# Performance work log

Hardware: AMD Instinct MI355X
Metric: run time of the kernel (lower is better)

## Reference

```python
import jax, jax.numpy as jnp
import numpy as np

FEATURES = [3, 64, 128, 256]
N_ITER = 5  # NNMF multiplicative-update iterations
K = 3
PAD = K // 2  # 'same' padding so spatial dims are preserved inside a block
EPS = 1e-20
BN_EPS = 1e-5


def conv2d(x, w, pad):
    # x: [B, Cin, H, W], w: [Cout, Cin, kh, kw] (torch OIHW layout)
    return jax.lax.conv_general_dilated(
        x, w, window_strides=(1, 1),
        padding=[(pad, pad), (pad, pad)],
        dimension_numbers=("NCHW", "OIHW", "NCHW"))


def nnmf_conv2d(x, w, n_iter, pad):
    # Non-negative, L1-normalized weights (per output filter)
    wp = jnp.abs(w)
    wn = wp / (wp.sum(axis=(1, 2, 3), keepdims=True) + EPS)
    # Input is non-negative (ReLU applied upstream); L1-normalize over channels
    x = x / (x.sum(axis=1, keepdims=True) + EPS)
    b, _, hh, ww = x.shape
    c_out = w.shape[0]
    # h init: uniform distribution over output channels
    h = jnp.full((b, c_out, hh, ww), 1.0 / c_out, dtype=x.dtype)
    # conv_transpose2d(h, W, padding=pad) == conv2d(h, flip(W).swap(O,I), padding=k-1-pad);
    # with odd k and pad = k//2 this is again 'same' padding.
    wt = jnp.transpose(jnp.flip(wn, (2, 3)), (1, 0, 2, 3))  # [Cin, Cout, kh, kw] as OIHW
    for _ in range(n_iter):
        recon = conv2d(h, wt, pad)                    # [B, Cin, H, W]
        h = h * conv2d(x / (recon + EPS), wn, pad)    # multiplicative update
        h = h / (h.sum(axis=1, keepdims=True) + EPS)  # renormalize over channels
    return h


def batchnorm(x, gamma, beta):
    # Training-mode BN: batch statistics over (N, H, W), biased variance
    mean = x.mean(axis=(0, 2, 3), keepdims=True)
    var = x.var(axis=(0, 2, 3), keepdims=True)
    xn = (x - mean) * jax.lax.rsqrt(var + BN_EPS)
    return xn * gamma[None, :, None, None] + beta[None, :, None, None]


def avgpool2(x):
    b, c, h, w = x.shape
    return x.reshape(b, c, h // 2, 2, w // 2, 2).mean(axis=(3, 5))


def block(x, w_nnmf, w_conv, b_conv, gamma, beta):
    x = jax.nn.relu(x)
    h = nnmf_conv2d(x, w_nnmf, N_ITER, PAD)
    y = conv2d(h, w_conv, 0) + b_conv[None, :, None, None]  # 1x1 conv
    y = jax.nn.relu(y)
    y = batchnorm(y, gamma, beta)
    return avgpool2(y)


def setup_inputs() -> dict:
    key = jax.random.key(0)
    keys = jax.random.split(key, 7)
    inp = {"x": jax.random.normal(keys[0], (16, 3, 128, 128), jnp.float32)}
    for i in range(3):
        cin, cout = FEATURES[i], FEATURES[i + 1]
        inp[f"w_nnmf{i}"] = jax.random.uniform(keys[1 + 2 * i], (cout, cin, K, K), jnp.float32)
        inp[f"w_conv{i}"] = jax.random.normal(keys[2 + 2 * i], (cout, cout, 1, 1), jnp.float32) / np.sqrt(cout).astype(np.float32)
        inp[f"b_conv{i}"] = jnp.zeros((cout,), jnp.float32)
        inp[f"gamma{i}"] = jnp.ones((cout,), jnp.float32)
        inp[f"beta{i}"] = jnp.zeros((cout,), jnp.float32)
    return inp


def reference(x, w_nnmf0, w_conv0, b_conv0, gamma0, beta0,
              w_nnmf1, w_conv1, b_conv1, gamma1, beta1,
              w_nnmf2, w_conv2, b_conv2, gamma2, beta2):
    x = block(x, w_nnmf0, w_conv0, b_conv0, gamma0, beta0)
    x = block(x, w_nnmf1, w_conv1, b_conv1, gamma1, beta1)
    x = block(x, w_nnmf2, w_conv2, b_conv2, gamma2, beta2)
    return x  # [16, 256, 16, 16]
```

## Files before the change

### kernel.cpp

```cpp
#include <hip/hip_runtime.h>

#define EPSV  1e-20f
#define BNEPS 1e-5f

typedef _Float16 f16x8 __attribute__((ext_vector_type(8)));
typedef _Float16 f16x4 __attribute__((ext_vector_type(4)));
typedef float    f32x4 __attribute__((ext_vector_type(4)));

__device__ inline unsigned pack2f16(float a, float b) {
    unsigned short ua = __builtin_bit_cast(unsigned short, (_Float16)a);
    unsigned short ub = __builtin_bit_cast(unsigned short, (_Float16)b);
    return ((unsigned)ub << 16) | ua;
}

template<int CIN, int COUT>
__global__ __launch_bounds__(256) void prep_w_f16_kernel(const float* __restrict__ w,
                                                         _Float16* __restrict__ wAh,
                                                         _Float16* __restrict__ wBh)
{
    const int co  = blockIdx.x;
    const int tid = threadIdx.x;
    const int N   = CIN * 9;
    const float* wrow = w + (size_t)co * N;

    float s = 0.f;
    for (int i = tid; i < N; i += 256) s += fabsf(wrow[i]);
    __shared__ float red[4];
    #pragma unroll
    for (int m = 32; m; m >>= 1) s += __shfl_xor(s, m, 64);
    if ((tid & 63) == 0) red[tid >> 6] = s;
    __syncthreads();
    s = red[0] + red[1] + red[2] + red[3];
    const float rn = 1.f / (s + EPSV);

    for (int i = tid; i < N; i += 256) {
        const int ci = i / 9, tap = i % 9;
        const int ky = tap / 3, kx = tap % 3;
        const float v = fabsf(wrow[i]) * rn;
        const int tf = (2 - ky) * 3 + (2 - kx);
        wBh[(((size_t)(ci >> 5) * 9 + tap) * COUT + co) * 32 + (ci & 31)] = (_Float16)v;
        wAh[(((size_t)(co >> 5) * 9 + tf) * CIN + ci) * 32 + (co & 31)] = (_Float16)v;
    }
}

__global__ __launch_bounds__(256) void zero_f16_kernel(_Float16* __restrict__ a, int n)
{
    const int i = blockIdx.x * 256 + threadIdx.x;
    if (i < n) a[i] = (_Float16)0.f;
}

__global__ __launch_bounds__(64) void prep_w0_kernel(const float* __restrict__ w,
                                                     _Float16* __restrict__ wA0h,
                                                     _Float16* __restrict__ wB0h)
{
    const int co = blockIdx.x, tid = threadIdx.x;
    float s = (tid < 27) ? fabsf(w[co * 27 + tid]) : 0.f;
    #pragma unroll
    for (int m = 32; m; m >>= 1) s += __shfl_xor(s, m, 64);
    const float rn = 1.f / (s + EPSV);
    if (tid < 27) {
        const int ci = tid / 9, tap = tid % 9, ky = tap / 3, kx = tap % 3;
        const float v = fabsf(w[co * 27 + tid]) * rn;
        const int tf = (2 - ky) * 3 + (2 - kx);
        wB0h[co * 64 + tap * 4 + ci] = (_Float16)v;
        wA0h[(((co >> 5) * 9 + tf) * 16 + ci) * 32 + (co & 31)] = (_Float16)v;
    }
}

__global__ __launch_bounds__(256) void prep_w1h_kernel(const float* __restrict__ w1,
                                                       _Float16* __restrict__ w1h, int n)
{
    const int i = blockIdx.x * 256 + threadIdx.x;
    if (i < n) w1h[i] = (_Float16)w1[i];
}

__global__ __launch_bounds__(256) void xn0_kernel(const float* __restrict__ x,
                                                  _Float16* __restrict__ xn4,
                                                  int npx, int HW)
{
    const int p = blockIdx.x * 256 + threadIdx.x;
    if (p >= npx) return;
    const int b = p / HW, r = p % HW;
    const float* ip = x + (size_t)b * 3 * HW + r;
    const float v0 = fmaxf(ip[0], 0.f), v1 = fmaxf(ip[HW], 0.f), v2 = fmaxf(ip[2 * HW], 0.f);
    const float rs = 1.f / (v0 + v1 + v2 + EPSV);
    unsigned* d = (unsigned*)(xn4 + (size_t)p * 4);
    d[0] = pack2f16(v0 * rs, v1 * rs);
    d[1] = pack2f16(v2 * rs, 0.f);
}

template<int ICg, int OCg, int NSPLIT, int OST, int NW, int NSIN,
         bool NORM_IN, bool UPDATE, bool FIRST>
__global__ __launch_bounds__(256, 1) void mfconv5(
    const _Float16* __restrict__ in, const _Float16* __restrict__ wgt,
    const _Float16* __restrict__ aux, _Float16* __restrict__ out,
    const float* __restrict__ Sin, float* __restrict__ Sout,
    int H, int W, int sstride)
{
    constexpr bool CSTAGE = FIRST && NORM_IN;
    constexpr int OCWG = OCg / NSPLIT;
    constexpr int NF = OCWG / 16;
    constexpr int HS = 18, WSp = 18, NSP = HS * WSp;
    constexpr int ICP = 40;
    constexpr int NCH = ICg / 32;
    constexpr int LS = (NSPLIT == 4) ? 2 : (NSPLIT == 2) ? 1 : 0;
    constexpr int NLD = NSP * 4;
    constexpr int IREG = (NLD + 255) / 256;
    constexpr int WOC = OCWG * 32;
    constexpr int NWLD = 9 * OCWG * 4;
    constexpr int WREG = (NWLD + 255) / 256;
    static_assert(OCWG % 16 == 0 && ICg % 32 == 0, "cfg");

    __shared__ _Float16 in_t[CSTAGE ? 1 : 2][NSP * ICP];
    __shared__ _Float16 w_t[2][9 * WOC];
    __shared__ float rS[(NORM_IN && !FIRST) ? NSP : 1];

    const int tid = threadIdx.x;
    const int lane = tid & 63, wave = tid >> 6;
    const int kq = lane >> 4, l15 = lane & 15;
    const int split = blockIdx.x & (NSPLIT - 1);
    const int tx = blockIdx.x >> LS;
    const int x0 = tx * 16, y0 = blockIdx.y * 16, b = blockIdx.z;
    const int HW = H * W;
    const int oc0 = split * OCWG;

    f16x8 ild[CSTAGE ? 1 : IREG];
    f16x8 wld[WREG];

    auto iload = [&](int kc) {
        #pragma unroll
        for (int r = 0; r < IREG; ++r) {
            const int i = tid + r * 256;
            f16x8 v = {0, 0, 0, 0, 0, 0, 0, 0};
            if (i < NLD) {
                const int sp = i >> 2, seg = i & 3;
                const int yy = y0 + sp / WSp - 1, xx = x0 + sp % WSp - 1;
                if (yy >= 0 && yy < H && xx >= 0 && xx < W)
                    v = __builtin_nontemporal_load((const f16x8*)(in +
                        ((size_t)b * HW + (size_t)yy * W + xx) * ICg + kc * 32 + seg * 8));
            }
            ild[r] = v;
        }
    };
    auto wload = [&](int kc) {
        #pragma unroll
        for (int r = 0; r < WREG; ++r) {
            const int j = tid + r * 256;
            if (j < NWLD) {
                const int tap = j / (OCWG * 4), rem = j % (OCWG * 4);
                const int oc = rem >> 2, e = rem & 3;
                wld[r] = *(const f16x8*)(wgt +
                    (((size_t)kc * 9 + tap) * OCg + oc0 + oc) * 32 + e * 8);
            }
        }
    };
    auto iwrite = [&](int buf) {
        #pragma unroll
        for (int r = 0; r < IREG; ++r) {
            const int i = tid + r * 256;
            if (i < NLD) {
                const int sp = i >> 2, seg = i & 3;
                if constexpr (NORM_IN && !FIRST) {
                    const float f = rS[sp];
                    unsigned* d = (unsigned*)&in_t[buf][sp * ICP + seg * 8];
                    d[0] = pack2f16((float)ild[r][0] * f, (float)ild[r][1] * f);
                    d[1] = pack2f16((float)ild[r][2] * f, (float)ild[r][3] * f);
                    d[2] = pack2f16((float)ild[r][4] * f, (float)ild[r][5] * f);
                    d[3] = pack2f16((float)ild[r][6] * f, (float)ild[r][7] * f);
                } else {
                    *(f16x8*)&in_t[buf][sp * ICP + seg * 8] = ild[r];
                }
            }
        }
    };
    auto wwrite = [&](int buf) {
        #pragma unroll
        for (int r = 0; r < WREG; ++r) {
            const int j = tid + r * 256;
            if (j < NWLD) {
                const int tap = j / (OCWG * 4), rem = j % (OCWG * 4);
                const int oc = rem >> 2, e = rem & 3;
                const int slot = e ^ ((oc >> 1) & 3);
                *(f16x8*)&w_t[buf][tap * WOC + oc * 32 + slot * 8] = wld[r];
            }
        }
    };

    const int prow = wave * 4;

    f32x4 acc[4][NF];
    #pragma unroll
    for (int mf = 0; mf < 4; ++mf)
        #pragma unroll
        for (int nf = 0; nf < NF; ++nf) acc[mf][nf] = (f32x4){0.f, 0.f, 0.f, 0.f};

    if constexpr (!CSTAGE) iload(0);
    wload(0);
    if constexpr (NORM_IN && !FIRST) {
        for (int i = tid; i < NSP; i += 256) {
            const int yy = y0 + i / WSp - 1, xx = x0 + i % WSp - 1;
            float sv = 0.f;
            if (yy >= 0 && yy < H && xx >= 0 && xx < W) {
                const size_t pix = (size_t)b * HW + (size_t)yy * W + xx;
                #pragma unroll
                for (int k = 0; k < NSIN; ++k) sv += Sin[(size_t)k * sstride + pix];
            }
            rS[i] = 1.f / (sv + EPSV);
        }
        __syncthreads();
    }
    if constexpr (CSTAGE) {
        const unsigned cpk = pack2f16(1.0f / (float)ICg, 1.0f / (float)ICg);
        for (int i = tid; i < NSP; i += 256) {
            const int yy = y0 + i / WSp - 1, xx = x0 + i % WSp - 1;
            const bool ok = (yy >= 0 && yy < H && xx >= 0 && xx < W);
            unsigned* d = (unsigned*)&in_t[0][i * ICP];
            #pragma unroll
            for (int seg = 0; seg < 16; ++seg) d[seg] = ok ? cpk : 0u;
        }
    } else {
        iwrite(0);
    }
    wwrite(0);
    __syncthreads();

    int cur = 0;
    for (int kc = 0; kc < NCH; ++kc) {
        if (kc + 1 < NCH) {
            if constexpr (!CSTAGE) iload(kc + 1);
            wload(kc + 1);
        }
        {
            const _Float16* ib = &in_t[CSTAGE ? 0 : cur][0];
            const _Float16* wb = &w_t[cur][0];
            #pragma unroll
            for (int dy = 0; dy < 3; ++dy) {
                #pragma unroll
                for (int dx = 0; dx < 3; ++dx) {
                    const int tap = dy * 3 + dx;
                    f16x8 bfr[NF];
                    #pragma unroll
                    for (int nf = 0; nf < NF; ++nf) {
                        const int oc = nf * 16 + l15;
                        bfr[nf] = *(const f16x8*)(
                            wb + tap * WOC + oc * 32 + (kq ^ ((oc >> 1) & 3)) * 8);
                    }
                    f16x8 afr[4];
                    #pragma unroll
                    for (int mf = 0; mf < 4; ++mf)
                        afr[mf] = *(const f16x8*)(
                            ib + ((prow + mf + dy) * WSp + l15 + dx) * ICP + kq * 8);
                    #pragma unroll
                    for (int mf = 0; mf < 4; ++mf)
                        #pragma unroll
                        for (int nf = 0; nf < NF; ++nf)
                            acc[mf][nf] = __builtin_amdgcn_mfma_f32_16x16x32_f16(
                                afr[mf], bfr[nf], acc[mf][nf], 0, 0, 0);
                }
            }
        }
        if (kc + 1 < NCH) {
            if constexpr (!CSTAGE) iwrite(cur ^ 1);
            wwrite(cur ^ 1);
            __syncthreads();
            cur ^= 1;
        }
    }

    #pragma unroll
    for (int mf = 0; mf < 4; ++mf) {
        const int gy = y0 + prow + mf;
        const size_t pixbase = (size_t)b * HW + (size_t)gy * W + x0 + kq * 4;
        if constexpr (!UPDATE) {
            #pragma unroll
            for (int nf = 0; nf < NF; ++nf) {
                const int oc = oc0 + nf * 16 + l15;
                if (oc < NW) {
                    #pragma unroll
                    for (int r = 0; r < 4; ++r) {
                        const size_t idx = (pixbase + r) * OST + oc;
                        out[idx] = (_Float16)((float)aux[idx] / (acc[mf][nf][r] + EPSV));
                    }
                }
            }
        } else {
            float s[4] = {0.f, 0.f, 0.f, 0.f};
            #pragma unroll
            for (int nf = 0; nf < NF; ++nf) {
                const int oc = oc0 + nf * 16 + l15;
                #pragma unroll
                for (int r = 0; r < 4; ++r) {
                    const size_t idx = (pixbase + r) * OST + oc;
                    float hv;
                    if constexpr (FIRST) hv = acc[mf][nf][r];
                    else                 hv = (float)out[idx] * acc[mf][nf][r];
                    const _Float16 hq = (_Float16)hv;
                    out[idx] = hq;
                    s[r] += (float)hq;
                }
            }
            #pragma unroll
            for (int mm = 1; mm < 16; mm <<= 1) {
                #pragma unroll
                for (int r = 0; r < 4; ++r) s[r] += __shfl_xor(s[r], mm);
            }
            if (l15 == 0) {
                float* sp_ = Sout + (size_t)split * sstride + pixbase;
                sp_[0] = s[0]; sp_[1] = s[1]; sp_[2] = s[2]; sp_[3] = s[3];
            }
        }
    }
}

template<bool FIRST>
__global__ __launch_bounds__(256) void mf0u_kernel(
    const _Float16* __restrict__ ratio4, const _Float16* __restrict__ wB0h,
    _Float16* __restrict__ h, float* __restrict__ Sout, int H, int W)
{
    constexpr int TW = 16;
    __shared__ _Float16 a_t[64 * 72];

    const int tid = threadIdx.x;
    const int lane = tid & 63, wave = tid >> 6;
    const int kq = lane >> 4, l15 = lane & 15;
    const int x0 = blockIdx.x * TW, y0 = blockIdx.y * 4, b = blockIdx.z;
    const int HW = H * W;

    for (int i = tid; i < 64 * 72 / 2; i += 256) ((unsigned*)a_t)[i] = 0;
    __syncthreads();
    for (int i = tid; i < 576; i += 256) {
        const int px = i / 9, tap = i % 9;
        const int py = px / TW, pxx = px % TW;
        const int yy = y0 + py + tap / 3 - 1, xx = x0 + pxx + tap % 3 - 1;
        if (yy >= 0 && yy < H && xx >= 0 && xx < W)
            *(f16x4*)&a_t[px * 72 + tap * 4] =
                *(const f16x4*)(ratio4 + ((size_t)b * HW + (size_t)yy * W + xx) * 4);
    }
    __syncthreads();

    f32x4 acc[4];
    #pragma unroll
    for (int nf = 0; nf < 4; ++nf) acc[nf] = (f32x4){0.f, 0.f, 0.f, 0.f};
    #pragma unroll
    for (int kc = 0; kc < 2; ++kc) {
        const f16x8 afr = *(const f16x8*)&a_t[(wave * 16 + l15) * 72 + kc * 32 + kq * 8];
        #pragma unroll
        for (int nf = 0; nf < 4; ++nf) {
            const f16x8 bfr = *(const f16x8*)(wB0h + (size_t)(nf * 16 + l15) * 64 + kc * 32 + kq * 8);
            acc[nf] = __builtin_amdgcn_mfma_f32_16x16x32_f16(afr, bfr, acc[nf], 0, 0, 0);
        }
    }

    const int pl = wave * 16 + kq * 4;
    const size_t pixbase = (size_t)b * HW + (size_t)(y0 + pl / TW) * W + x0 + pl % TW;
    float s[4] = {0.f, 0.f, 0.f, 0.f};
    #pragma unroll
    for (int nf = 0; nf < 4; ++nf) {
        const int oc = nf * 16 + l15;
        #pragma unroll
        for (int r = 0; r < 4; ++r) {
            const size_t idx = (pixbase + r) * 64 + oc;
            float hv;
            if constexpr (FIRST) hv = acc[nf][r];
            else                 hv = (float)h[idx] * acc[nf][r];
            const _Float16 hq = (_Float16)hv;
            h[idx] = hq;
            s[r] += (float)hq;
        }
    }
    #pragma unroll
    for (int mm = 1; mm < 16; mm <<= 1) {
        #pragma unroll
        for (int r = 0; r < 4; ++r) s[r] += __shfl_xor(s[r], mm);
    }
    if (l15 == 0) {
        float* sp_ = Sout + pixbase;
        sp_[0] = s[0]; sp_[1] = s[1]; sp_[2] = s[2]; sp_[3] = s[3];
    }
}

template<int C, int MODE, int NSIN>
__global__ __launch_bounds__(256) void posty_kernel(
    const _Float16* __restrict__ h, const float* __restrict__ S,
    const _Float16* __restrict__ w1h, const float* __restrict__ bias,
    const float* __restrict__ bnst, float* __restrict__ part,
    void* __restrict__ outp, int H, int W, int sst)
{
    constexpr int NF = C / 16, CP = C + 8;
    __shared__ _Float16 a_t[64 * CP];
    __shared__ float rs_t[64];
    __shared__ float sred1[MODE == 0 ? 4 * C : 1];
    __shared__ float sred2[MODE == 0 ? 4 * C : 1];
    __shared__ float pool_t[MODE == 1 ? 16 * (C + 1) : 1];

    const int tid = threadIdx.x;
    const int lane = tid & 63, wave = tid >> 6;
    const int kq = lane >> 4, l15 = lane & 15;
    const int WT = W / 32;
    const int tx = blockIdx.x % WT, ty = blockIdx.x / WT;
    const int b = blockIdx.y;
    const int HW = H * W;

    if (tid < 64) {
        const int gp = (2 * ty + (tid >> 5)) * W + tx * 32 + (tid & 31);
        float sv = 0.f;
        #pragma unroll
        for (int k = 0; k < NSIN; ++k) sv += S[(size_t)k * sst + (size_t)b * HW + gp];
        rs_t[tid] = 1.f / (sv + EPSV);
    }
    __syncthreads();
    for (int i = tid; i < 64 * (C / 8); i += 256) {
        const int sp = i / (C / 8), seg = i % (C / 8);
        const int gp = (2 * ty + (sp >> 5)) * W + tx * 32 + (sp & 31);
        const f16x8 v = *(const f16x8*)(h + ((size_t)b * HW + gp) * C + seg * 8);
        const float f = rs_t[sp];
        unsigned* d = (unsigned*)&a_t[sp * CP + seg * 8];
        d[0] = pack2f16((float)v[0] * f, (float)v[1] * f);
        d[1] = pack2f16((float)v[2] * f, (float)v[3] * f);
        d[2] = pack2f16((float)v[4] * f, (float)v[5] * f);
        d[3] = pack2f16((float)v[6] * f, (float)v[7] * f);
    }
    __syncthreads();

    f32x4 acc[NF];
    #pragma unroll
    for (int nf = 0; nf < NF; ++nf) acc[nf] = (f32x4){0.f, 0.f, 0.f, 0.f};
    #pragma unroll
    for (int kc = 0; kc < C / 32; ++kc) {
        const f16x8 afr = *(const f16x8*)&a_t[(wave * 16 + l15) * CP + kc * 32 + kq * 8];
        #pragma unroll
        for (int nf = 0; nf < NF; ++nf) {
            const f16x8 bfr = *(const f16x8*)(w1h + (size_t)(nf * 16 + l15) * C + kc * 32 + kq * 8);
            acc[nf] = __builtin_amdgcn_mfma_f32_16x16x32_f16(afr, bfr, acc[nf], 0, 0, 0);
        }
    }

    const int pl = wave * 16 + kq * 4;

    if constexpr (MODE == 0) {
        const int wgid = b * gridDim.x + blockIdx.x;
        #pragma unroll
        for (int nf = 0; nf < NF; ++nf) {
            const int oc = nf * 16 + l15;
            const float bv = bias[oc];
            float s1 = 0.f, s2 = 0.f;
            #pragma unroll
            for (int r = 0; r < 4; ++r) {
                const float y = fmaxf(acc[nf][r] + bv, 0.f);
                s1 += y; s2 += y * y;
            }
            s1 += __shfl_xor(s1, 16); s2 += __shfl_xor(s2, 16);
            s1 += __shfl_xor(s1, 32); s2 += __shfl_xor(s2, 32);
            if (kq == 0) {
                sred1[wave * C + oc] = s1;
                sred2[wave * C + oc] = s2;
            }
        }
        __syncthreads();
        for (int oc = tid; oc < C; oc += 256) {
            const float s1 = sred1[oc] + sred1[C + oc] + sred1[2 * C + oc] + sred1[3 * C + oc];
            const float s2 = sred2[oc] + sred2[C + oc] + sred2[2 * C + oc] + sred2[3 * C + oc];
            part[((size_t)wgid * C + oc) * 2 + 0] = s1;
            part[((size_t)wgid * C + oc) * 2 + 1] = s2;
        }
    } else {
        __syncthreads();
        #pragma unroll
        for (int nf = 0; nf < NF; ++nf) {
            const int oc = nf * 16 + l15;
            const float bv = bias[oc];
            #pragma unroll
            for (int r = 0; r < 4; ++r)
                a_t[(pl + r) * CP + oc] = (_Float16)fmaxf(acc[nf][r] + bv, 0.f);
        }
        __syncthreads();
        const int Wo = W >> 1;
        if constexpr (MODE == 2) {
            for (int i = tid; i < 16 * C; i += 256) {
                const int ox = i % 16, c = i / 16;
                const float y00 = (float)a_t[(2 * ox) * CP + c];
                const float y01 = (float)a_t[(2 * ox + 1) * CP + c];
                const float y10 = (float)a_t[(32 + 2 * ox) * CP + c];
                const float y11 = (float)a_t[(32 + 2 * ox + 1) * CP + c];
                const float v = (y00 + y01 + y10 + y11) * 0.25f * bnst[c] + bnst[C + c];
                ((float*)outp)[(((size_t)b * C + c) * (size_t)(H >> 1) + ty) * Wo + tx * 16 + ox] = v;
            }
        } else {
            for (int i = tid; i < 16 * C; i += 256) {
                const int ox = i / C, c = i % C;
                const float y00 = (float)a_t[(2 * ox) * CP + c];
                const float y01 = (float)a_t[(2 * ox + 1) * CP + c];
                const float y10 = (float)a_t[(32 + 2 * ox) * CP + c];
                const float y11 = (float)a_t[(32 + 2 * ox + 1) * CP + c];
                pool_t[ox * (C + 1) + c] =
                    fmaxf((y00 + y01 + y10 + y11) * 0.25f * bnst[c] + bnst[C + c], 0.f);
            }
            __syncthreads();
            const int px = tid >> 4, prt = tid & 15;
            float ps = 0.f;
            for (int c = prt; c < C; c += 16) ps += pool_t[px * (C + 1) + c];
            ps += __shfl_xor(ps, 1); ps += __shfl_xor(ps, 2);
            ps += __shfl_xor(ps, 4); ps += __shfl_xor(ps, 8);
            const float rs = 1.f / (ps + EPSV);
            _Float16* xo = (_Float16*)outp;
            const size_t obase = ((size_t)b * (HW >> 2) + (size_t)ty * Wo + tx * 16 + px) * C;
            for (int c = prt; c < C; c += 16)
                xo[obase + c] = (_Float16)(pool_t[px * (C + 1) + c] * rs);
        }
    }
}

template<int C>
__global__ __launch_bounds__(256) void stats_kernel(const float* __restrict__ part, int nwg, float invM,
                                                    const float* __restrict__ gamma,
                                                    const float* __restrict__ beta,
                                                    float* __restrict__ stats)
{
    const int oc = blockIdx.x;
    const int tid = threadIdx.x;
    float s1 = 0.f, s2 = 0.f;
    for (int w = tid; w < nwg; w += 256) {
        s1 += part[((size_t)w * C + oc) * 2 + 0];
        s2 += part[((size_t)w * C + oc) * 2 + 1];
    }
    __shared__ float r1[4], r2[4];
    #pragma unroll
    for (int m = 32; m; m >>= 1) { s1 += __shfl_xor(s1, m, 64); s2 += __shfl_xor(s2, m, 64); }
    if ((tid & 63) == 0) { r1[tid >> 6] = s1; r2[tid >> 6] = s2; }
    __syncthreads();
    if (tid == 0) {
        s1 = r1[0] + r1[1] + r1[2] + r1[3];
        s2 = r2[0] + r2[1] + r2[2] + r2[3];
        const float mean = s1 * invM;
        const float var  = s2 * invM - mean * mean;
        const float rstd = rsqrtf(var + BNEPS);
        const float scale = gamma[oc] * rstd;
        stats[oc]     = scale;
        stats[C + oc] = beta[oc] - mean * scale;
    }
}

extern "C" void kernel_launch(void* const* d_in, const int* in_sizes, int n_in,
                              void* d_out, int out_size, void* d_ws, size_t ws_size,
                              hipStream_t stream)
{
    const float* x = (const float*)d_in[0];
    float* ws      = (float*)d_ws;
    float* S       = ws;
    float* part    = S + 262144;
    float* bnstats = part + 1048576;
    _Float16* h      = (_Float16*)(bnstats + 512);
    _Float16* xnh    = h + 16777216;
    _Float16* ratioh = xnh + 4194304;
    _Float16* wAh    = ratioh + 4194304;
    _Float16* wBh    = wAh + 294912;
    _Float16* w1h    = wBh + 294912;
    _Float16* wA0h   = w1h + 65536;
    _Float16* wB0h   = wA0h + 9216;

    const int B = 16;

    {
        const int H = 128, W = 128, HW = H * W, npx = B * HW;
        zero_f16_kernel<<<(9216 + 255) / 256, 256, 0, stream>>>(wA0h, 9216);
        prep_w0_kernel<<<64, 64, 0, stream>>>((const float*)d_in[1], wA0h, wB0h);
        xn0_kernel<<<npx / 256, 256, 0, stream>>>(x, xnh, npx, HW);
        mfconv5<64, 16, 1, 4, 4, 1, true, false, true>
            <<<dim3(8, 8, B), 256, 0, stream>>>(h, wA0h, xnh, ratioh, S, nullptr, H, W, npx);
        mf0u_kernel<true><<<dim3(8, 32, B), 256, 0, stream>>>(ratioh, wB0h, h, S, H, W);
        for (int it = 1; it < 5; ++it) {
            mfconv5<64, 16, 1, 4, 4, 1, true, false, false>
                <<<dim3(8, 8, B), 256, 0, stream>>>(h, wA0h, xnh, ratioh, S, nullptr, H, W, npx);
            mf0u_kernel<false><<<dim3(8, 32, B), 256, 0, stream>>>(ratioh, wB0h, h, S, H, W);
        }
        prep_w1h_kernel<<<16, 256, 0, stream>>>((const float*)d_in[2], w1h, 64 * 64);
        dim3 pg((W / 32) * (H / 2), B);
        posty_kernel<64, 0, 1><<<pg, 256, 0, stream>>>(h, S, w1h, (const float*)d_in[3],
                                                       nullptr, part, nullptr, H, W, npx);
        stats_kernel<64><<<64, 256, 0, stream>>>(part, pg.x * pg.y, 1.0f / (float)npx,
                                                 (const float*)d_in[4], (const float*)d_in[5], bnstats);
        posty_kernel<64, 1, 1><<<pg, 256, 0, stream>>>(h, S, w1h, (const float*)d_in[3],
                                                       bnstats, nullptr, xnh, H, W, npx);
    }

    {
        const int H = 64, W = 64, HW = H * W, npx = B * HW;
        prep_w_f16_kernel<64, 128><<<128, 256, 0, stream>>>((const float*)d_in[6], wAh, wBh);
        mfconv5<128, 64, 1, 64, 64, 1, true, false, true>
            <<<dim3(4, 4, B), 256, 0, stream>>>(h, wAh, xnh, ratioh, S, nullptr, H, W, npx);
        mfconv5<64, 128, 2, 128, 128, 1, false, true, true>
            <<<dim3(8, 4, B), 256, 0, stream>>>(ratioh, wBh, nullptr, h, nullptr, S, H, W, npx);
        for (int it = 1; it < 5; ++it) {
            mfconv5<128, 64, 1, 64, 64, 2, true, false, false>
                <<<dim3(4, 4, B), 256, 0, stream>>>(h, wAh, xnh, ratioh, S, nullptr, H, W, npx);
            mfconv5<64, 128, 2, 128, 128, 1, false, true, false>
                <<<dim3(8, 4, B), 256, 0, stream>>>(ratioh, wBh, nullptr, h, nullptr, S, H, W, npx);
        }
        prep_w1h_kernel<<<64, 256, 0, stream>>>((const float*)d_in[7], w1h, 128 * 128);
        dim3 pg((W / 32) * (H / 2), B);
        posty_kernel<128, 0, 2><<<pg, 256, 0, stream>>>(h, S, w1h, (const float*)d_in[8],
                                                        nullptr, part, nullptr, H, W, npx);
        stats_kernel<128><<<128, 256, 0, stream>>>(part, pg.x * pg.y, 1.0f / (float)npx,
                                                   (const float*)d_in[9], (const float*)d_in[10], bnstats);
        posty_kernel<128, 1, 2><<<pg, 256, 0, stream>>>(h, S, w1h, (const float*)d_in[8],
                                                        bnstats, nullptr, xnh, H, W, npx);
    }

    {
        const int H = 32, W = 32, HW = H * W, npx = B * HW;
        prep_w_f16_kernel<128, 256><<<256, 256, 0, stream>>>((const float*)d_in[11], wAh, wBh);
        mfconv5<256, 128, 4, 128, 128, 1, true, false, true>
            <<<dim3(8, 2, B), 256, 0, stream>>>(h, wAh, xnh, ratioh, S, nullptr, H, W, npx);
        mfconv5<128, 256, 4, 256, 256, 1, false, true, true>
            <<<dim3(8, 2, B), 256, 0, stream>>>(ratioh, wBh, nullptr, h, nullptr, S, H, W, npx);
        for (int it = 1; it < 5; ++it) {
            mfconv5<256, 128, 4, 128, 128, 4, true, false, false>
                <<<dim3(8, 2, B), 256, 0, stream>>>(h, wAh, xnh, ratioh, S, nullptr, H, W, npx);
            mfconv5<128, 256, 4, 256, 256, 1, false, true, false>
                <<<dim3(8, 2, B), 256, 0, stream>>>(ratioh, wBh, nullptr, h, nullptr, S, H, W, npx);
        }
        prep_w1h_kernel<<<256, 256, 0, stream>>>((const float*)d_in[12], w1h, 256 * 256);
        dim3 pg((W / 32) * (H / 2), B);
        posty_kernel<256, 0, 4><<<pg, 256, 0, stream>>>(h, S, w1h, (const float*)d_in[13],
                                                        nullptr, part, nullptr, H, W, npx);
        stats_kernel<256><<<256, 256, 0, stream>>>(part, pg.x * pg.y, 1.0f / (float)npx,
                                                   (const float*)d_in[14], (const float*)d_in[15], bnstats);
        posty_kernel<256, 2, 4><<<pg, 256, 0, stream>>>(h, S, w1h, (const float*)d_in[13],
                                                        bnstats, nullptr, d_out, H, W, npx);
    }
}
```

Measured before the change: 824.7 us.

## Fuse NNMF reconstruction and update convs into one halo-tiled kernel per iteration

Adds mffuse_kernel, which computes the reconstruction conv over a 20x20 haloed tile, forms the ratio x/recon in LDS, then runs the update conv and h renormalisation sums in the same kernel. This removes the ratio round-trip through global memory and halves launches for blocks 0 and 1. It also merges all weight preparation into one kernel and changes the block-2 reconstruction split. The cost is recomputing recon on the halo ring, plus heavy LDS and register use at one block per CU.

```diff
diff --git a/kernel.cpp b/kernel.cpp
--- a/kernel.cpp
+++ b/kernel.cpp
@@ -13,26 +13,20 @@
     return ((unsigned)ub << 16) | ua;
 }
 
-template<int CIN, int COUT>
-__global__ __launch_bounds__(256) void prep_w_f16_kernel(const float* __restrict__ w,
-                                                         _Float16* __restrict__ wAh,
-                                                         _Float16* __restrict__ wBh)
+__device__ __forceinline__ void prep_generic(const float* __restrict__ w, int CIN, int COUT,
+                                             _Float16* __restrict__ wAh, _Float16* __restrict__ wBh,
+                                             int co, int tid, float* red)
 {
-    const int co  = blockIdx.x;
-    const int tid = threadIdx.x;
-    const int N   = CIN * 9;
+    const int N = CIN * 9;
     const float* wrow = w + (size_t)co * N;
-
     float s = 0.f;
     for (int i = tid; i < N; i += 256) s += fabsf(wrow[i]);
-    __shared__ float red[4];
     #pragma unroll
     for (int m = 32; m; m >>= 1) s += __shfl_xor(s, m, 64);
     if ((tid & 63) == 0) red[tid >> 6] = s;
     __syncthreads();
     s = red[0] + red[1] + red[2] + red[3];
     const float rn = 1.f / (s + EPSV);
-
     for (int i = tid; i < N; i += 256) {
         const int ci = i / 9, tap = i % 9;
         const int ky = tap / 3, kx = tap % 3;
@@ -43,35 +37,51 @@
     }
 }
 
-__global__ __launch_bounds__(256) void zero_f16_kernel(_Float16* __restrict__ a, int n)
+__global__ __launch_bounds__(256) void prep_all_kernel(
+    const float* __restrict__ w0,  const float* __restrict__ w1_0,
+    const float* __restrict__ wb1, const float* __restrict__ w1_1,
+    const float* __restrict__ wb2, const float* __restrict__ w1_2,
+    _Float16* __restrict__ wA0h, _Float16* __restrict__ wB0h,
+    _Float16* __restrict__ wA1h, _Float16* __restrict__ wB1h,
+    _Float16* __restrict__ wA2h, _Float16* __restrict__ wB2h,
+    _Float16* __restrict__ w1h0, _Float16* __restrict__ w1h1, _Float16* __restrict__ w1h2)
 {
-    const int i = blockIdx.x * 256 + threadIdx.x;
-    if (i < n) a[i] = (_Float16)0.f;
-}
-
-__global__ __launch_bounds__(64) void prep_w0_kernel(const float* __restrict__ w,
-                                                     _Float16* __restrict__ wA0h,
-                                                     _Float16* __restrict__ wB0h)
-{
-    const int co = blockIdx.x, tid = threadIdx.x;
-    float s = (tid < 27) ? fabsf(w[co * 27 + tid]) : 0.f;
-    #pragma unroll
-    for (int m = 32; m; m >>= 1) s += __shfl_xor(s, m, 64);
-    const float rn = 1.f / (s + EPSV);
-    if (tid < 27) {
-        const int ci = tid / 9, tap = tid % 9, ky = tap / 3, kx = tap % 3;
-        const float v = fabsf(w[co * 27 + tid]) * rn;
-        const int tf = (2 - ky) * 3 + (2 - kx);
-        wB0h[co * 64 + tap * 4 + ci] = (_Float16)v;
-        wA0h[(((co >> 5) * 9 + tf) * 16 + ci) * 32 + (co & 31)] = (_Float16)v;
-    }
-}
-
-__global__ __launch_bounds__(256) void prep_w1h_kernel(const float* __restrict__ w1,
-                                                       _Float16* __restrict__ w1h, int n)
-{
-    const int i = blockIdx.x * 256 + threadIdx.x;
-    if (i < n) w1h[i] = (_Float16)w1[i];
+    __shared__ float red[4];
+    const int bid = blockIdx.x, tid = threadIdx.x;
+    if (bid < 64) {
+        const int co = bid;
+        float s = (tid < 27) ? fabsf(w0[co * 27 + tid]) : 0.f;
+        #pragma unroll
+        for (int m = 32; m; m >>= 1) s += __shfl_xor(s, m, 64);
+        if ((tid & 63) == 0) red[tid >> 6] = s;
+        __syncthreads();
+        s = red[0] + red[1] + red[2] + red[3];
+        const float rn = 1.f / (s + EPSV);
+        for (int i = tid; i < 9 * 32; i += 256) {
+            const int tap = i / 32, ci = i % 32;
+            const float v = (ci < 3) ? fabsf(w0[co * 27 + ci * 9 + tap]) * rn : 0.f;
+            wB0h[((size_t)tap * 64 + co) * 32 + ci] = (_Float16)v;
+        }
+        for (int i = tid; i < 9 * 16; i += 256) {
+            const int tf = i / 16, ci = i % 16;
+            float v = 0.f;
+            if (ci < 3) {
+                const int tap = (2 - tf / 3) * 3 + (2 - tf % 3);
+                v = fabsf(w0[co * 27 + ci * 9 + tap]) * rn;
+            }
+            wA0h[((((size_t)(co >> 5) * 9 + tf) * 16 + ci) * 32) + (co & 31)] = (_Float16)v;
+        }
+    } else if (bid < 192) {
+        prep_generic(wb1, 64, 128, wA1h, wB1h, bid - 64, tid, red);
+    } else if (bid < 448) {
+        prep_generic(wb2, 128, 256, wA2h, wB2h, bid - 192, tid, red);
+    } else if (bid < 464) {
+        const int i = (bid - 448) * 256 + tid; w1h0[i] = (_Float16)w1_0[i];
+    } else if (bid < 528) {
+        const int i = (bid - 464) * 256 + tid; w1h1[i] = (_Float16)w1_1[i];
+    } else {
+        const int i = (bid - 528) * 256 + tid; w1h2[i] = (_Float16)w1_2[i];
+    }
 }
 
 __global__ __launch_bounds__(256) void xn0_kernel(const float* __restrict__ x,
@@ -87,6 +97,310 @@
     unsigned* d = (unsigned*)(xn4 + (size_t)p * 4);
     d[0] = pack2f16(v0 * rs, v1 * rs);
     d[1] = pack2f16(v2 * rs, 0.f);
+}
+
+template<int COUT, int CINP, int NFA, int NPO, int XST, int XNC, bool FIRST>
+__global__ __launch_bounds__(256, 1) void mffuse_kernel(
+    _Float16* __restrict__ h, const _Float16* __restrict__ wA,
+    const _Float16* __restrict__ wB, const _Float16* __restrict__ xn,
+    float* __restrict__ S, int H, int W)
+{
+    constexpr int OCA  = NFA * 16;
+    constexpr int NCHA = COUT / 32;
+    constexpr int NCHB = CINP / 32;
+    constexpr int OCP  = COUT / NPO;
+    constexpr int NFB  = OCP / 16;
+    constexpr int NPIECES = NPO * NCHB;
+    constexpr int ICPH = 40;
+    constexpr int NSPA = 400;
+    constexpr int ICP2 = CINP + 8;
+    constexpr int NRPX = 324;
+    constexpr int PIECE = 9 * OCP * 32;
+    constexpr int WRS0  = 9 * OCA * 32;
+    constexpr int IRS = (16000 > PIECE) ? 16000 : PIECE;
+    constexpr int WRS = (NPIECES > 1 && PIECE > WRS0) ? PIECE : WRS0;
+    constexpr int NLDA = NSPA * 4;
+    constexpr int IREGA = (NLDA + 255) / 256;
+    constexpr int NWLA = 9 * OCA * 4;
+    constexpr int WREGA = (NWLA + 255) / 256;
+    constexpr int NWLB = PIECE / 8;
+    constexpr int WREGB = (NWLB + 255) / 256;
+
+    __shared__ float rS_s[NSPA];
+    __shared__ _Float16 lds_I[IRS];
+    __shared__ _Float16 lds_W[WRS];
+    __shared__ _Float16 lds_R[NRPX * ICP2];
+
+    const int tid = threadIdx.x;
+    const int lane = tid & 63, wave = tid >> 6;
+    const int kq = lane >> 4, l15 = lane & 15;
+    const int x0 = blockIdx.x * 16, y0 = blockIdx.y * 16, b = blockIdx.z;
+    const int HW = H * W;
+
+    f16x8 ild[IREGA];
+    f16x8 wla[WREGA];
+    f16x8 wlb[WREGB];
+
+    auto iloadA = [&](int kc) {
+        #pragma unroll
+        for (int r = 0; r < IREGA; ++r) {
+            const int i = tid + r * 256;
+            f16x8 v = {0, 0, 0, 0, 0, 0, 0, 0};
+            if (i < NLDA) {
+                const int sp = i >> 2, seg = i & 3;
+                const int yy = y0 + sp / 20 - 2, xx = x0 + sp % 20 - 2;
+                if (yy >= 0 && yy < H && xx >= 0 && xx < W)
+                    v = __builtin_nontemporal_load((const f16x8*)(h +
+                        ((size_t)b * HW + (size_t)yy * W + xx) * COUT + kc * 32 + seg * 8));
+            }
+            ild[r] = v;
+        }
+    };
+    auto iwriteA = [&]() {
+        #pragma unroll
+        for (int r = 0; r < IREGA; ++r) {
+            const int i = tid + r * 256;
+            if (i < NLDA) {
+                const int sp = i >> 2, seg = i & 3;
+                const float f = rS_s[sp];
+                unsigned* d = (unsigned*)&lds_I[sp * ICPH + seg * 8];
+                d[0] = pack2f16((float)ild[r][0] * f, (float)ild[r][1] * f);
+                d[1] = pack2f16((float)ild[r][2] * f, (float)ild[r][3] * f);
+                d[2] = pack2f16((float)ild[r][4] * f, (float)ild[r][5] * f);
+                d[3] = pack2f16((float)ild[r][6] * f, (float)ild[r][7] * f);
+            }
+        }
+    };
+    auto wloadA = [&](int kc) {
+        #pragma unroll
+        for (int r = 0; r < WREGA; ++r) {
+            const int j = tid + r * 256;
+            if (j < NWLA) {
+                const int tap = j / (OCA * 4), rem = j % (OCA * 4);
+                const int oc = rem >> 2, e = rem & 3;
+                wla[r] = *(const f16x8*)(wA + (((size_t)kc * 9 + tap) * OCA + oc) * 32 + e * 8);
+            }
+        }
+    };
+    auto wwriteA = [&]() {
+        #pragma unroll
+        for (int r = 0; r < WREGA; ++r) {
+            const int j = tid + r * 256;
+            if (j < NWLA) {
+                const int tap = j / (OCA * 4), rem = j % (OCA * 4);
+                const int oc = rem >> 2, e = rem & 3;
+                const int slot = e ^ ((oc >> 1) & 3);
+                *(f16x8*)&lds_W[tap * (OCA * 32) + oc * 32 + slot * 8] = wla[r];
+            }
+        }
+    };
+    auto wloadB = [&](int p) {
+        const int oh = p / NCHB, kc = p % NCHB;
+        #pragma unroll
+        for (int r = 0; r < WREGB; ++r) {
+            const int j = tid + r * 256;
+            if (j < NWLB) {
+                const int tap = j / (OCP * 4), rem = j % (OCP * 4);
+                const int oc = rem >> 2, e = rem & 3;
+                wlb[r] = *(const f16x8*)(wB +
+                    (((size_t)kc * 9 + tap) * COUT + oh * OCP + oc) * 32 + e * 8);
+            }
+        }
+    };
+    auto wwriteB = [&](int p) {
+        _Float16* dst = (p & 1) ? lds_W : lds_I;
+        #pragma unroll
+        for (int r = 0; r < WREGB; ++r) {
+            const int j = tid + r * 256;
+            if (j < NWLB) {
+                const int tap = j / (OCP * 4), rem = j % (OCP * 4);
+                const int oc = rem >> 2, e = rem & 3;
+                const int slot = e ^ ((oc >> 1) & 3);
+                *(f16x8*)&dst[tap * (OCP * 32) + oc * 32 + slot * 8] = wlb[r];
+            }
+        }
+    };
+
+    int ryj[6], rxj[6];
+    bool vj[6];
+    #pragma unroll
+    for (int j = 0; j < 6; ++j) {
+        const int f = wave + 4 * j;
+        vj[j] = (f < 21);
+        const int p = f * 16 + l15;
+        const int pc = (p < NRPX) ? p : (NRPX - 1);
+        ryj[j] = pc / 18; rxj[j] = pc % 18;
+    }
+
+    f32x4 racc[6][NFA];
+    #pragma unroll
+    for (int j = 0; j < 6; ++j)
+        #pragma unroll
+        for (int nfa = 0; nfa < NFA; ++nfa) racc[j][nfa] = (f32x4){0.f, 0.f, 0.f, 0.f};
+
+    if constexpr (!FIRST) iloadA(0);
+    wloadA(0);
+    if constexpr (XNC < CINP) {
+        for (int i = tid; i < NRPX * ICP2 / 2; i += 256) ((unsigned*)lds_R)[i] = 0u;
+    }
+    if constexpr (!FIRST) {
+        for (int i = tid; i < NSPA; i += 256) {
+            const int yy = y0 + i / 20 - 2, xx = x0 + i % 20 - 2;
+            float sv = 0.f;
+            if (yy >= 0 && yy < H && xx >= 0 && xx < W)
+                sv = S[(size_t)b * HW + (size_t)yy * W + xx];
+            rS_s[i] = 1.f / (sv + EPSV);
+        }
+        __syncthreads();
+        iwriteA();
+    } else {
+        const unsigned cpk = pack2f16(1.f / (float)COUT, 1.f / (float)COUT);
+        for (int i = tid; i < NSPA; i += 256) {
+            const int yy = y0 + i / 20 - 2, xx = x0 + i % 20 - 2;
+            const bool ok = (yy >= 0 && yy < H && xx >= 0 && xx < W);
+            unsigned* d = (unsigned*)&lds_I[i * ICPH];
+            #pragma unroll
+            for (int sg = 0; sg < 16; ++sg) d[sg] = ok ? cpk : 0u;
+        }
+    }
+    wwriteA();
+    __syncthreads();
+
+    for (int kc = 0; kc < NCHA; ++kc) {
+        if (kc + 1 < NCHA) {
+            if constexpr (!FIRST) iloadA(kc + 1);
+            wloadA(kc + 1);
+        }
+        #pragma unroll
+        for (int tap = 0; tap < 9; ++tap) {
+            const int dy = tap / 3, dx = tap % 3;
+            f16x8 bfr[NFA];
+            #pragma unroll
+            for (int nfa = 0; nfa < NFA; ++nfa) {
+                const int oc = nfa * 16 + l15;
+                bfr[nfa] = *(const f16x8*)&lds_W[tap * (OCA * 32) + oc * 32 + (kq ^ ((oc >> 1) & 3)) * 8];
+            }
+            #pragma unroll
+            for (int j = 0; j < 6; ++j) {
+                if (vj[j]) {
+                    const f16x8 afr = *(const f16x8*)&lds_I[((ryj[j] + dy) * 20 + rxj[j] + dx) * ICPH + kq * 8];
+                    #pragma unroll
+                    for (int nfa = 0; nfa < NFA; ++nfa)
+                        racc[j][nfa] = __builtin_amdgcn_mfma_f32_16x16x32_f16(afr, bfr[nfa], racc[j][nfa], 0, 0, 0);
+                }
+            }
+        }
+        if (kc + 1 < NCHA) {
+            __syncthreads();
+            if constexpr (!FIRST) iwriteA();
+            wwriteA();
+            __syncthreads();
+        }
+    }
+
+    wloadB(0);
+    #pragma unroll
+    for (int j = 0; j < 6; ++j) {
+        if (!vj[j]) continue;
+        const int f = wave + 4 * j;
+        #pragma unroll
+        for (int r = 0; r < 4; ++r) {
+            const int p = f * 16 + kq * 4 + r;
+            if (p < NRPX) {
+                const int ry = p / 18, rx = p % 18;
+                const int gy = y0 - 1 + ry, gx = x0 - 1 + rx;
+                const bool ok = (gy >= 0 && gy < H && gx >= 0 && gx < W);
+                #pragma unroll
+                for (int nfa = 0; nfa < NFA; ++nfa) {
+                    const int oc = nfa * 16 + l15;
+                    float rv = 0.f;
+                    if (ok && oc < XNC) {
+                        const size_t pb = (size_t)b * HW + (size_t)gy * W + gx;
+                        rv = (float)xn[pb * XST + oc] / (racc[j][nfa][r] + EPSV);
+                    }
+                    lds_R[p * ICP2 + oc] = (_Float16)rv;
+                }
+            }
+        }
+    }
+    __syncthreads();
+    wwriteB(0);
+    __syncthreads();
+
+    const int prow = wave * 4;
+    float ssum[4][4];
+    #pragma unroll
+    for (int mf = 0; mf < 4; ++mf)
+        #pragma unroll
+        for (int r = 0; r < 4; ++r) ssum[mf][r] = 0.f;
+
+    for (int oh = 0; oh < NPO; ++oh) {
+        f32x4 uacc[4][NFB];
+        #pragma unroll
+        for (int mf = 0; mf < 4; ++mf)
+            #pragma unroll
+            for (int nfb = 0; nfb < NFB; ++nfb) uacc[mf][nfb] = (f32x4){0.f, 0.f, 0.f, 0.f};
+
+        for (int kc = 0; kc < NCHB; ++kc) {
+            const int p = oh * NCHB + kc;
+            if (p + 1 < NPIECES) wloadB(p + 1);
+            const _Float16* wpb = (p & 1) ? lds_W : lds_I;
+            #pragma unroll
+            for (int tap = 0; tap < 9; ++tap) {
+                const int dy = tap / 3, dx = tap % 3;
+                f16x8 bfr[NFB];
+                #pragma unroll
+                for (int nfb = 0; nfb < NFB; ++nfb) {
+                    const int oc = nfb * 16 + l15;
+                    bfr[nfb] = *(const f16x8*)&wpb[tap * (OCP * 32) + oc * 32 + (kq ^ ((oc >> 1) & 3)) * 8];
+                }
+                #pragma unroll
+                for (int mf = 0; mf < 4; ++mf) {
+                    const f16x8 afr = *(const f16x8*)&lds_R[((prow + mf + dy) * 18 + l15 + dx) * ICP2 + kc * 32 + kq * 8];
+                    #pragma unroll
+                    for (int nfb = 0; nfb < NFB; ++nfb)
+                        uacc[mf][nfb] = __builtin_amdgcn_mfma_f32_16x16x32_f16(afr, bfr[nfb], uacc[mf][nfb], 0, 0, 0);
+                }
+            }
+            if (p + 1 < NPIECES) {
+                __syncthreads();
+                wwriteB(p + 1);
+                __syncthreads();
+            }
+        }
+        #pragma unroll
+        for (int mf = 0; mf < 4; ++mf) {
+            const int gy = y0 + prow + mf;
+            const size_t pixbase = (size_t)b * HW + (size_t)gy * W + x0 + kq * 4;
+            #pragma unroll
+            for (int nfb = 0; nfb < NFB; ++nfb) {
+                const int oc = oh * OCP + nfb * 16 + l15;
+                #pragma unroll
+                for (int r = 0; r < 4; ++r) {
+                    const size_t idx = (pixbase + r) * COUT + oc;
+                    float hv;
+                    if constexpr (FIRST) hv = uacc[mf][nfb][r];
+                    else                 hv = (float)h[idx] * uacc[mf][nfb][r];
+                    const _Float16 hq = (_Float16)hv;
+                    h[idx] = hq;
+                    ssum[mf][r] += (float)hq;
+                }
+            }
+        }
+    }
+    #pragma unroll
+    for (int mf = 0; mf < 4; ++mf) {
+        #pragma unroll
+        for (int r = 0; r < 4; ++r) {
+            float v = ssum[mf][r];
+            v += __shfl_xor(v, 1); v += __shfl_xor(v, 2);
+            v += __shfl_xor(v, 4); v += __shfl_xor(v, 8);
+            if (l15 == 0) {
+                const int gy = y0 + prow + mf;
+                S[(size_t)b * HW + (size_t)gy * W + x0 + kq * 4 + r] = v;
+            }
+        }
+    }
 }
 
 template<int ICg, int OCg, int NSPLIT, int OST, int NW, int NSIN,
@@ -312,73 +626,6 @@
     }
 }
 
-template<bool FIRST>
-__global__ __launch_bounds__(256) void mf0u_kernel(
-    const _Float16* __restrict__ ratio4, const _Float16* __restrict__ wB0h,
-    _Float16* __restrict__ h, float* __restrict__ Sout, int H, int W)
-{
-    constexpr int TW = 16;
-    __shared__ _Float16 a_t[64 * 72];
-
-    const int tid = threadIdx.x;
-    const int lane = tid & 63, wave = tid >> 6;
-    const int kq = lane >> 4, l15 = lane & 15;
-    const int x0 = blockIdx.x * TW, y0 = blockIdx.y * 4, b = blockIdx.z;
-    const int HW = H * W;
-
-    for (int i = tid; i < 64 * 72 / 2; i += 256) ((unsigned*)a_t)[i] = 0;
-    __syncthreads();
-    for (int i = tid; i < 576; i += 256) {
-        const int px = i / 9, tap = i % 9;
-        const int py = px / TW, pxx = px % TW;
-        const int yy = y0 + py + tap / 3 - 1, xx = x0 + pxx + tap % 3 - 1;
-        if (yy >= 0 && yy < H && xx >= 0 && xx < W)
-            *(f16x4*)&a_t[px * 72 + tap * 4] =
-                *(const f16x4*)(ratio4 + ((size_t)b * HW + (size_t)yy * W + xx) * 4);
-    }
-    __syncthreads();
-
-    f32x4 acc[4];
-    #pragma unroll
-    for (int nf = 0; nf < 4; ++nf) acc[nf] = (f32x4){0.f, 0.f, 0.f, 0.f};
-    #pragma unroll
-    for (int kc = 0; kc < 2; ++kc) {
-        const f16x8 afr = *(const f16x8*)&a_t[(wave * 16 + l15) * 72 + kc * 32 + kq * 8];
-        #pragma unroll
-        for (int nf = 0; nf < 4; ++nf) {
-            const f16x8 bfr = *(const f16x8*)(wB0h + (size_t)(nf * 16 + l15) * 64 + kc * 32 + kq * 8);
-            acc[nf] = __builtin_amdgcn_mfma_f32_16x16x32_f16(afr, bfr, acc[nf], 0, 0, 0);
-        }
-    }
-
-    const int pl = wave * 16 + kq * 4;
-    const size_t pixbase = (size_t)b * HW + (size_t)(y0 + pl / TW) * W + x0 + pl % TW;
-    float s[4] = {0.f, 0.f, 0.f, 0.f};
-    #pragma unroll
-    for (int nf = 0; nf < 4; ++nf) {
-        const int oc = nf * 16 + l15;
-        #pragma unroll
-        for (int r = 0; r < 4; ++r) {
-            const size_t idx = (pixbase + r) * 64 + oc;
-            float hv;
-            if constexpr (FIRST) hv = acc[nf][r];
-            else                 hv = (float)h[idx] * acc[nf][r];
-            const _Float16 hq = (_Float16)hv;
-            h[idx] = hq;
-            s[r] += (float)hq;
-        }
-    }
-    #pragma unroll
-    for (int mm = 1; mm < 16; mm <<= 1) {
-        #pragma unroll
-        for (int r = 0; r < 4; ++r) s[r] += __shfl_xor(s[r], mm);
-    }
-    if (l15 == 0) {
-        float* sp_ = Sout + pixbase;
-        sp_[0] = s[0]; sp_[1] = s[1]; sp_[2] = s[2]; sp_[3] = s[3];
-    }
-}
-
 template<int C, int MODE, int NSIN>
 __global__ __launch_bounds__(256) void posty_kernel(
     const _Float16* __restrict__ h, const float* __restrict__ S,
@@ -552,80 +799,75 @@
     _Float16* h      = (_Float16*)(bnstats + 512);
     _Float16* xnh    = h + 16777216;
     _Float16* ratioh = xnh + 4194304;
-    _Float16* wAh    = ratioh + 4194304;
-    _Float16* wBh    = wAh + 294912;
-    _Float16* w1h    = wBh + 294912;
-    _Float16* wA0h   = w1h + 65536;
+    _Float16* wA1h   = ratioh + 4194304;
+    _Float16* wB1h   = wA1h + 73728;
+    _Float16* wA2h   = wB1h + 73728;
+    _Float16* wB2h   = wA2h + 294912;
+    _Float16* w1h0   = wB2h + 294912;
+    _Float16* w1h1   = w1h0 + 4096;
+    _Float16* w1h2   = w1h1 + 16384;
+    _Float16* wA0h   = w1h2 + 65536;
     _Float16* wB0h   = wA0h + 9216;
 
     const int B = 16;
+
+    prep_all_kernel<<<784, 256, 0, stream>>>(
+        (const float*)d_in[1], (const float*)d_in[2],
+        (const float*)d_in[6], (const float*)d_in[7],
+        (const float*)d_in[11], (const float*)d_in[12],
+        wA0h, wB0h, wA1h, wB1h, wA2h, wB2h, w1h0, w1h1, w1h2);
 
     {
         const int H = 128, W = 128, HW = H * W, npx = B * HW;
-        zero_f16_kernel<<<(9216 + 255) / 256, 256, 0, stream>>>(wA0h, 9216);
-        prep_w0_kernel<<<64, 64, 0, stream>>>((const float*)d_in[1], wA0h, wB0h);
         xn0_kernel<<<npx / 256, 256, 0, stream>>>(x, xnh, npx, HW);
-        mfconv5<64, 16, 1, 4, 4, 1, true, false, true>
-            <<<dim3(8, 8, B), 256, 0, stream>>>(h, wA0h, xnh, ratioh, S, nullptr, H, W, npx);
-        mf0u_kernel<true><<<dim3(8, 32, B), 256, 0, stream>>>(ratioh, wB0h, h, S, H, W);
-        for (int it = 1; it < 5; ++it) {
-            mfconv5<64, 16, 1, 4, 4, 1, true, false, false>
-                <<<dim3(8, 8, B), 256, 0, stream>>>(h, wA0h, xnh, ratioh, S, nullptr, H, W, npx);
-            mf0u_kernel<false><<<dim3(8, 32, B), 256, 0, stream>>>(ratioh, wB0h, h, S, H, W);
-        }
-        prep_w1h_kernel<<<16, 256, 0, stream>>>((const float*)d_in[2], w1h, 64 * 64);
+        mffuse_kernel<64, 32, 1, 1, 4, 4, true>
+            <<<dim3(8, 8, B), 256, 0, stream>>>(h, wA0h, wB0h, xnh, S, H, W);
+        for (int it = 1; it < 5; ++it)
+            mffuse_kernel<64, 32, 1, 1, 4, 4, false>
+                <<<dim3(8, 8, B), 256, 0, stream>>>(h, wA0h, wB0h, xnh, S, H, W);
         dim3 pg((W / 32) * (H / 2), B);
-        posty_kernel<64, 0, 1><<<pg, 256, 0, stream>>>(h, S, w1h, (const float*)d_in[3],
+        posty_kernel<64, 0, 1><<<pg, 256, 0, stream>>>(h, S, w1h0, (const float*)d_in[3],
                                                        nullptr, part, nullptr, H, W, npx);
         stats_kernel<64><<<64, 256, 0, stream>>>(part, pg.x * pg.y, 1.0f / (float)npx,
                                                  (const float*)d_in[4], (const float*)d_in[5], bnstats);
-        posty_kernel<64, 1, 1><<<pg, 256, 0, stream>>>(h, S, w1h, (const float*)d_in[3],
+        posty_kernel<64, 1, 1><<<pg, 256, 0, stream>>>(h, S, w1h0, (const float*)d_in[3],
                                                        bnstats, nullptr, xnh, H, W, npx);
     }
 
     {
         const int H = 64, W = 64, HW = H * W, npx = B * HW;
-        prep_w_f16_kernel<64, 128><<<128, 256, 0, stream>>>((const float*)d_in[6], wAh, wBh);
-        mfconv5<128, 64, 1, 64, 64, 1, true, false, true>
-            <<<dim3(4, 4, B), 256, 0, stream>>>(h, wAh, xnh, ratioh, S, nullptr, H, W, npx);
-        mfconv5<64, 128, 2, 128, 128, 1, false, true, true>
-            <<<dim3(8, 4, B), 256, 0, stream>>>(ratioh, wBh, nullptr, h, nullptr, S, H, W, npx);
-        for (int it = 1; it < 5; ++it) {
-            mfconv5<128, 64, 1, 64, 64, 2, true, false, false>
-                <<<dim3(4, 4, B), 256, 0, stream>>>(h, wAh, xnh, ratioh, S, nullptr, H, W, npx);
-            mfconv5<64, 128, 2, 128, 128, 1, false, true, false>
-                <<<dim3(8, 4, B), 256, 0, stream>>>(ratioh, wBh, nullptr, h, nullptr, S, H, W, npx);
-        }
-        prep_w1h_kernel<<<64, 256, 0, stream>>>((const float*)d_in[7], w1h, 128 * 128);
+        mffuse_kernel<128, 64, 4, 2, 64, 64, true>
+            <<<dim3(4, 4, B), 256, 0, stream>>>(h, wA1h, wB1h, xnh, S, H, W);
+        for (int it = 1; it < 5; ++it)
+            mffuse_kernel<128, 64, 4, 2, 64, 64, false>
+                <<<dim3(4, 4, B), 256, 0, stream>>>(h, wA1h, wB1h, xnh, S, H, W);
         dim3 pg((W / 32) * (H / 2), B);
-        posty_kernel<128, 0, 2><<<pg, 256, 0, stream>>>(h, S, w1h, (const float*)d_in[8],
+        posty_kernel<128, 0, 1><<<pg, 256, 0, stream>>>(h, S, w1h1, (const float*)d_in[8],
                                                         nullptr, part, nullptr, H, W, npx);
         stats_kernel<128><<<128, 256, 0, stream>>>(part, pg.x * pg.y, 1.0f / (float)npx,
                                                    (const float*)d_in[9], (const float*)d_in[10], bnstats);
-        posty_kernel<128, 1, 2><<<pg, 256, 0, stream>>>(h, S, w1h, (const float*)d_in[8],
+        posty_kernel<128, 1, 1><<<pg, 256, 0, stream>>>(h, S, w1h1, (const float*)d_in[8],
                                                         bnstats, nullptr, xnh, H, W, npx);
     }
 
     {
         const int H = 32, W = 32, HW = H * W, npx = B * HW;
-        prep_w_f16_kernel<128, 256><<<256, 256, 0, stream>>>((const float*)d_in[11], wAh, wBh);
-        mfconv5<256, 128, 4, 128, 128, 1, true, false, true>
-            <<<dim3(8, 2, B), 256, 0, stream>>>(h, wAh, xnh, ratioh, S, nullptr, H, W, npx);
+        mfconv5<256, 128, 2, 128, 128, 1, true, false, true>
+            <<<dim3(4, 2, B), 256, 0, stream>>>(h, wA2h, xnh, ratioh, S, nullptr, H, W, npx);
         mfconv5<128, 256, 4, 256, 256, 1, false, true, true>
-            <<<dim3(8, 2, B), 256, 0, stream>>>(ratioh, wBh, nullptr, h, nullptr, S, H, W, npx);
+            <<<dim3(8, 2, B), 256, 0, stream>>>(ratioh, wB2h, nullptr, h, nullptr, S, H, W, npx);
         for (int it = 1; it < 5; ++it) {
-            mfconv5<256, 128, 4, 128, 128, 4, true, false, false>
-                <<<dim3(8, 2, B), 256, 0, stream>>>(h, wAh, xnh, ratioh, S, nullptr, H, W, npx);
+            mfconv5<256, 128, 2, 128, 128, 4, true, false, false>
+                <<<dim3(4, 2, B), 256, 0, stream>>>(h, wA2h, xnh, ratioh, S, nullptr, H, W, npx);
             mfconv5<128, 256, 4, 256, 256, 1, false, true, false>
-                <<<dim3(8, 2, B), 256, 0, stream>>>(ratioh, wBh, nullptr, h, nullptr, S, H, W, npx);
-        }
-        prep_w1h_kernel<<<256, 256, 0, stream>>>((const float*)d_in[12], w1h, 256 * 256);
+                <<<dim3(8, 2, B), 256, 0, stream>>>(ratioh, wB2h, nullptr, h, nullptr, S, H, W, npx);
+        }
         dim3 pg((W / 32) * (H / 2), B);
-        posty_kernel<256, 0, 4><<<pg, 256, 0, stream>>>(h, S, w1h, (const float*)d_in[13],
+        posty_kernel<256, 0, 4><<<pg, 256, 0, stream>>>(h, S, w1h2, (const float*)d_in[13],
                                                         nullptr, part, nullptr, H, W, npx);
         stats_kernel<256><<<256, 256, 0, stream>>>(part, pg.x * pg.y, 1.0f / (float)npx,
                                                    (const float*)d_in[14], (const float*)d_in[15], bnstats);
-        posty_kernel<256, 2, 4><<<pg, 256, 0, stream>>>(h, S, w1h, (const float*)d_in[13],
+        posty_kernel<256, 2, 4><<<pg, 256, 0, stream>>>(h, S, w1h2, (const float*)d_in[13],
                                                         bnstats, nullptr, d_out, H, W, npx);
     }
 }
```

New measurement: 995.2 us. +20.7%, slower.
